# Kernel tuning notes

Hardware: AMD Instinct MI355X
Metric: run time of the kernel (lower is better)

Reference implementation:

```python
import jax, jax.numpy as jnp
import numpy as np

B, N, C = 4, 2048, 1024
H = 16
HD = C // H  # 64
THETA = 10000.0


def setup_inputs() -> dict:
    key = jax.random.key(0)
    k1, k2, k3, k4 = jax.random.split(key, 4)
    x = jax.random.normal(k1, (B, N, C), dtype=jnp.float32)
    # Linear-style init scaling to keep activations sane
    w_qkv = jax.random.normal(k2, (3 * C, C), dtype=jnp.float32) * (1.0 / np.sqrt(C))
    w_proj = jax.random.normal(k3, (C, C), dtype=jnp.float32) * (1.0 / np.sqrt(C))
    b_proj = jax.random.normal(k4, (C,), dtype=jnp.float32) * 0.01
    # RoPE frequencies: freqs_cis[n, j] = exp(i * n * theta^(-2j/hd))
    inv_freq = 1.0 / (THETA ** (jnp.arange(0, HD, 2, dtype=jnp.float32) / HD))  # (HD/2,)
    angles = jnp.arange(N, dtype=jnp.float32)[:, None] * inv_freq[None, :]  # (N, HD/2)
    freqs_cos = jnp.cos(angles)
    freqs_sin = jnp.sin(angles)
    return {"x": x, "w_qkv": w_qkv, "w_proj": w_proj, "b_proj": b_proj,
            "freqs_cos": freqs_cos, "freqs_sin": freqs_sin}


def _apply_rope(t, cos, sin):
    # t: (B, N, H, HD) -> complex pairs on last dim
    tr = t.reshape(t.shape[:-1] + (HD // 2, 2))
    a, b = tr[..., 0], tr[..., 1]
    c = cos[None, :, None, :]  # (1, N, 1, HD/2)
    s = sin[None, :, None, :]
    out = jnp.stack([a * c - b * s, a * s + b * c], axis=-1)
    return out.reshape(t.shape)


def reference(x, w_qkv, w_proj, b_proj, freqs_cos, freqs_sin):
    Bx, Nx, Cx = x.shape
    scale = HD ** -0.5
    qkv = jnp.einsum('bnc,dc->bnd', x, w_qkv)  # (B, N, 3C)
    qkv = qkv.reshape(Bx, Nx, 3, H, HD)
    q, k, v = qkv[:, :, 0], qkv[:, :, 1], qkv[:, :, 2]  # (B, N, H, HD)
    q = _apply_rope(q, freqs_cos, freqs_sin)
    k = _apply_rope(k, freqs_cos, freqs_sin)
    # (B, H, N, HD)
    q = q.transpose(0, 2, 1, 3)
    k = k.transpose(0, 2, 1, 3)
    v = v.transpose(0, 2, 1, 3)
    attn = jnp.einsum('bhnd,bhmd->bhnm', q, k) * scale
    attn = jax.nn.softmax(attn, axis=-1)
    out = jnp.einsum('bhnm,bhmd->bhnd', attn, v)  # (B, H, N, HD)
    out = out.transpose(0, 2, 1, 3).reshape(Bx, Nx, Cx)
    return jnp.einsum('bnc,dc->bnd', out, w_proj) + b_proj
```

## Files before the change

### kernel.cpp

```cpp
#include <hip/hip_runtime.h>
#include <hip/hip_bf16.h>
#include <stdint.h>

#define B_  4
#define N_  2048
#define C_  1024
#define H_  16
#define HD_ 64
#define M_  (B_*N_)
#define K3_ (3*C_)

typedef __bf16 bf16;
typedef __bf16 bf16x8 __attribute__((ext_vector_type(8)));
typedef __bf16 bf16x4 __attribute__((ext_vector_type(4)));
typedef float f32x4 __attribute__((ext_vector_type(4)));
typedef float f32x16 __attribute__((ext_vector_type(16)));

#if __has_builtin(__builtin_amdgcn_exp2f)
#define EXP2(x) __builtin_amdgcn_exp2f(x)
#else
#define EXP2(x) exp2f(x)
#endif

__global__ void castk3(const float* __restrict__ a, bf16* __restrict__ oa, int na4,
                       const float* __restrict__ b, bf16* __restrict__ ob, int nb4,
                       const float* __restrict__ c, bf16* __restrict__ oc, int nc4) {
    int total = na4 + nb4 + nc4;
    int stride = gridDim.x * blockDim.x;
    for (int i = blockIdx.x * blockDim.x + threadIdx.x; i < total; i += stride) {
        const float* src; bf16* dst; int j = i;
        if (j < na4)              { src = a; dst = oa; }
        else if ((j -= na4) < nb4){ src = b; dst = ob; }
        else                      { j -= nb4; src = c; dst = oc; }
        float4 v = reinterpret_cast<const float4*>(src)[j];
        bf16x4 o;
        o[0] = (bf16)v.x; o[1] = (bf16)v.y; o[2] = (bf16)v.z; o[3] = (bf16)v.w;
        *reinterpret_cast<bf16x4*>(dst + (size_t)j * 4) = o;
    }
}

__device__ __forceinline__ void gll16(const bf16* g, const bf16* l) {
    __builtin_amdgcn_global_load_lds(
        (const __attribute__((address_space(1))) void*)g,
        (__attribute__((address_space(3))) void*)l, 16, 0, 0);
}

__device__ __forceinline__ uint32_t pkbf(float a, float b) {
    union { bf16 h[2]; uint32_t u; } U;
    U.h[0] = (bf16)a; U.h[1] = (bf16)b;
    return U.u;
}

__device__ __forceinline__ uint32_t pkraw(bf16 a, bf16 b) {
    union { bf16 h[2]; uint32_t u; } U;
    U.h[0] = a; U.h[1] = b;
    return U.u;
}

template<int MODE>
__global__ __launch_bounds__(256, 4)
void gemm_bt(const bf16* __restrict__ A, const bf16* __restrict__ Bm,
             int Nn, int Kk,
             bf16* __restrict__ qout, bf16* __restrict__ kout, bf16* __restrict__ vout,
             const float* __restrict__ fcos, const float* __restrict__ fsin,
             const float* __restrict__ bias, float* __restrict__ Cout)
{
    __shared__ bf16 a_lds[2][128 * 32];
    __shared__ bf16 b_lds[2][128 * 32];
    const int tid  = threadIdx.x;
    const int lane = tid & 63;
    const int w    = tid >> 6;
    const int wr   = w >> 1, wc = w & 1;
    const int ntile = Nn >> 7;
    const int nwg = gridDim.x, cpx = nwg >> 3;
    const int swz = (blockIdx.x & 7) * cpx + (blockIdx.x >> 3);
    const int bx = swz % ntile, by = swz / ntile;
    const int m0 = by * 128, n0 = bx * 128;

    f32x4 acc[4][4] = {};

    const int c0 = tid, c1 = tid + 256;
    const bf16* ga0 = A  + (size_t)(m0 + (c0 >> 2)) * Kk + (c0 & 3) * 8;
    const bf16* ga1 = A  + (size_t)(m0 + (c1 >> 2)) * Kk + (c1 & 3) * 8;
    const bf16* gb0 = Bm + (size_t)(n0 + (c0 >> 2)) * Kk + (c0 & 3) * 8;
    const bf16* gb1 = Bm + (size_t)(n0 + (c1 >> 2)) * Kk + (c1 & 3) * 8;

    const int rA = lane & 15;
    const int kk = (lane >> 4) * 8;

    gll16(ga0, &a_lds[0][w * 512]);
    gll16(ga1, &a_lds[0][w * 512 + 2048]);
    gll16(gb0, &b_lds[0][w * 512]);
    gll16(gb1, &b_lds[0][w * 512 + 2048]);
    __syncthreads();

    for (int k0 = 0; k0 < Kk; k0 += 32) {
        const int cur = (k0 >> 5) & 1, nxt = cur ^ 1;
        if (k0 + 32 < Kk) {
            gll16(ga0 + k0 + 32, &a_lds[nxt][w * 512]);
            gll16(ga1 + k0 + 32, &a_lds[nxt][w * 512 + 2048]);
            gll16(gb0 + k0 + 32, &b_lds[nxt][w * 512]);
            gll16(gb1 + k0 + 32, &b_lds[nxt][w * 512 + 2048]);
        }

        bf16x8 af[4], bfr[4];
#pragma unroll
        for (int m = 0; m < 4; ++m)
            af[m] = *reinterpret_cast<const bf16x8*>(&a_lds[cur][(wr * 64 + m * 16 + rA) * 32 + kk]);
#pragma unroll
        for (int n = 0; n < 4; ++n)
            bfr[n] = *reinterpret_cast<const bf16x8*>(&b_lds[cur][(wc * 64 + n * 16 + rA) * 32 + kk]);
#pragma unroll
        for (int m = 0; m < 4; ++m)
#pragma unroll
            for (int n = 0; n < 4; ++n)
                acc[m][n] = __builtin_amdgcn_mfma_f32_16x16x32_bf16(af[m], bfr[n], acc[m][n], 0, 0, 0);
        __syncthreads();
    }

    if (MODE == 1) {
#pragma unroll
        for (int n = 0; n < 4; ++n) {
            int cg = n0 + wc * 64 + n * 16 + (lane & 15);
            float bv = bias[cg];
#pragma unroll
            for (int m = 0; m < 4; ++m) {
                int rg = m0 + wr * 64 + m * 16 + (lane >> 4) * 4;
#pragma unroll
                for (int r = 0; r < 4; ++r)
                    Cout[(size_t)(rg + r) * Nn + cg] = acc[m][n][r] + bv;
            }
        }
    } else {
        const int part = n0 >> 10;
#pragma unroll
        for (int n = 0; n < 4; ++n) {
            int cg  = n0 + wc * 64 + n * 16 + (lane & 15);
            int rem = cg & 1023;
            int h   = rem >> 6, hd = rem & 63;
#pragma unroll
            for (int m = 0; m < 4; ++m) {
#pragma unroll
                for (int r = 0; r < 4; ++r) {
                    int rg   = m0 + wr * 64 + m * 16 + (lane >> 4) * 4 + r;
                    int b    = rg >> 11, nrow = rg & 2047;
                    float val = acc[m][n][r];
                    size_t oi = ((size_t)(b * 16 + h) * N_ + nrow) * HD_ + hd;
                    if (part == 2) {
                        vout[oi] = (bf16)val;
                    } else {
                        float p   = __shfl_xor(val, 1);
                        float cth = fcos[nrow * 32 + (hd >> 1)];
                        float sth = fsin[nrow * 32 + (hd >> 1)];
                        float o   = (lane & 1) ? (val * cth + p * sth) : (val * cth - p * sth);
                        if (part == 0) { o *= 0.18033688011112042f; qout[oi] = (bf16)o; }
                        else           { kout[oi] = (bf16)o; }
                    }
                }
            }
        }
    }
}

#define NT_ (N_ / 64)
__global__ __launch_bounds__(256, 2)
void attn_kernel(const bf16* __restrict__ Q, const bf16* __restrict__ Kb,
                 const bf16* __restrict__ Vb, bf16* __restrict__ Ob)
{
    __shared__ bf16 k_lds[2][64 * 64];
    __shared__ bf16 vt_lds[2][64 * 64];
    const int tid = threadIdx.x, lane = tid & 63, w = tid >> 6;
    const int h5  = lane >> 5;
    const int l31 = lane & 31;
    const int nqt = N_ / 128;
    const int cpx = gridDim.x >> 3;
    const int swzb = (blockIdx.x & 7) * cpx + (blockIdx.x >> 3);
    const int bh = swzb / nqt, qt = swzb % nqt;
    const size_t base = (size_t)bh * N_ * HD_;
    const int q0 = qt * 128 + w * 32;

    bf16x8 qf[4];
    {
        const bf16* qp = Q + base + (size_t)(q0 + l31) * HD_ + h5 * 8;
#pragma unroll
        for (int t = 0; t < 4; ++t)
            qf[t] = *reinterpret_cast<const bf16x8*>(qp + t * 16);
    }

    f32x16 oT[2] = {};
    float l_run = 0.f;

    const int kRowA = tid >> 3;
    const int kColA = ((tid & 7) ^ (kRowA & 7)) * 8;
    const int kRowB = kRowA + 32;
    const int kColB = ((tid & 7) ^ (kRowB & 7)) * 8;
    const bf16* kSrcA = Kb + base + (size_t)kRowA * HD_ + kColA;
    const bf16* kSrcB = Kb + base + (size_t)kRowB * HD_ + kColB;

    const int kp = tid & 31, dc = tid >> 5;
    const bf16* vSrc0 = Vb + base + (size_t)(2 * kp) * HD_ + dc * 8;
    const bf16* vSrc1 = vSrc0 + HD_;

#define STORE_VT(bufidx, va, vb) do {                                              \
        char* vtb = reinterpret_cast<char*>(&vt_lds[0][0]) + (bufidx) * 8192;      \
        _Pragma("unroll")                                                          \
        for (int j = 0; j < 8; ++j) {                                              \
            int byteoff = (dc * 8 + j) * 128 + ((4 * kp) ^ (j << 4));              \
            *reinterpret_cast<uint32_t*>(vtb + byteoff) = pkraw((va)[j], (vb)[j]); \
        }                                                                          \
    } while (0)

    bf16x8 v0 = *reinterpret_cast<const bf16x8*>(vSrc0);
    bf16x8 v1 = *reinterpret_cast<const bf16x8*>(vSrc1);
    gll16(kSrcA, &k_lds[0][w * 512]);
    gll16(kSrcB, &k_lds[0][2048 + w * 512]);
    STORE_VT(0, v0, v1);
    __syncthreads();

    for (int it = 0; it < NT_; ++it) {
        const int cur = it & 1, nxt = cur ^ 1;
        const bool more = (it + 1 < NT_);

        if (more) {
            size_t adv = (size_t)(it + 1) * 64 * HD_;
            v0 = *reinterpret_cast<const bf16x8*>(vSrc0 + adv);
            v1 = *reinterpret_cast<const bf16x8*>(vSrc1 + adv);
            gll16(kSrcA + adv, &k_lds[nxt][w * 512]);
            gll16(kSrcB + adv, &k_lds[nxt][2048 + w * 512]);
        }

        const char* kbase  = reinterpret_cast<const char*>(&k_lds[0][0]) + cur * 8192;
        const char* vtbase = reinterpret_cast<const char*>(&vt_lds[0][0]) + cur * 8192;
        float psum = 0.f;

#pragma unroll
        for (int s = 0; s < 2; ++s) {
            f32x16 st = {};
            const int row = s * 32 + l31;
#pragma unroll
            for (int t = 0; t < 4; ++t) {
                int cc = (2 * t + h5) ^ (row & 7);
                bf16x8 kf = *reinterpret_cast<const bf16x8*>(kbase + row * 128 + cc * 16);
                st = __builtin_amdgcn_mfma_f32_32x32x16_bf16(kf, qf[t], st, 0, 0, 0);
            }

#pragma unroll
            for (int i = 0; i < 16; ++i)
                st[i] = EXP2(st[i]);

            float t8[8];
#pragma unroll
            for (int i = 0; i < 8; ++i) t8[i] = st[i] + st[i + 8];
#pragma unroll
            for (int i = 0; i < 4; ++i) t8[i] = t8[i] + t8[i + 4];
            psum += (t8[0] + t8[1]) + (t8[2] + t8[3]);

            uint32_t pk2[4][2];
#pragma unroll
            for (int g = 0; g < 4; ++g) {
                pk2[g][0] = pkbf(st[4 * g + 0], st[4 * g + 1]);
                pk2[g][1] = pkbf(st[4 * g + 2], st[4 * g + 3]);
            }
#pragma unroll
            for (int tt = 0; tt < 2; ++tt) {
                const int t = 2 * s + tt;
                uint32_t a0 = pk2[2 * tt][0], b0 = pk2[2 * tt + 1][0];
                uint32_t a1 = pk2[2 * tt][1], b1 = pk2[2 * tt + 1][1];
                asm volatile("v_permlane32_swap_b32 %0, %1" : "+v"(a0), "+v"(b0));
                asm volatile("v_permlane32_swap_b32 %0, %1" : "+v"(a1), "+v"(b1));
                union { uint32_t u[4]; bf16x8 v; } U;
                U.u[0] = a0; U.u[1] = a1; U.u[2] = b0; U.u[3] = b1;
#pragma unroll
                for (int n = 0; n < 2; ++n) {
                    int vrow = n * 32 + l31;
                    int cc   = (2 * t + h5) ^ (vrow & 7);
                    bf16x8 vf = *reinterpret_cast<const bf16x8*>(vtbase + vrow * 128 + cc * 16);
                    oT[n] = __builtin_amdgcn_mfma_f32_32x32x16_bf16(vf, U.v, oT[n], 0, 0, 0);
                }
            }

            if (s == 0 && more) STORE_VT(nxt, v0, v1);
        }

        psum += __shfl_xor(psum, 32);
        l_run += psum;

        __syncthreads();
    }

    const int b = bh >> 4, hh = bh & 15;
    float inv = 1.0f / l_run;
    int q = q0 + l31;
#pragma unroll
    for (int n = 0; n < 2; ++n)
#pragma unroll
        for (int g = 0; g < 4; ++g) {
            int d = n * 32 + 8 * g + 4 * h5;
            bf16x4 o4;
#pragma unroll
            for (int r = 0; r < 4; ++r) o4[r] = (bf16)(oT[n][4 * g + r] * inv);
            *reinterpret_cast<bf16x4*>(Ob + ((size_t)(b * N_ + q)) * C_ + hh * 64 + d) = o4;
        }
#undef STORE_VT
}

extern "C" void kernel_launch(void* const* d_in, const int* in_sizes, int n_in,
                              void* d_out, int out_size, void* d_ws, size_t ws_size,
                              hipStream_t stream) {
    const float* x     = (const float*)d_in[0];
    const float* wqkv  = (const float*)d_in[1];
    const float* wproj = (const float*)d_in[2];
    const float* bproj = (const float*)d_in[3];
    const float* fcos  = (const float*)d_in[4];
    const float* fsin  = (const float*)d_in[5];
    float* out = (float*)d_out;

    bf16* x_bf     = (bf16*)d_ws;
    bf16* wqkv_bf  = x_bf    + (size_t)M_ * C_;
    bf16* wproj_bf = wqkv_bf + (size_t)K3_ * C_;
    bf16* qbuf     = wproj_bf + (size_t)C_ * C_;
    bf16* kbuf     = qbuf  + (size_t)M_ * C_;
    bf16* vbuf     = kbuf  + (size_t)M_ * C_;
    bf16* abuf     = vbuf  + (size_t)M_ * C_;

    castk3<<<2048, 256, 0, stream>>>(x,     x_bf,     M_ * C_ / 4,
                                     wqkv,  wqkv_bf,  K3_ * C_ / 4,
                                     wproj, wproj_bf, C_ * C_ / 4);

    gemm_bt<0><<<64 * 24, 256, 0, stream>>>(x_bf, wqkv_bf, K3_, C_,
                                            qbuf, kbuf, vbuf, fcos, fsin, nullptr, nullptr);
    attn_kernel<<<64 * 16, 256, 0, stream>>>(qbuf, kbuf, vbuf, abuf);
    gemm_bt<1><<<64 * 8, 256, 0, stream>>>(abuf, wproj_bf, C_, C_,
                                           nullptr, nullptr, nullptr, nullptr, nullptr, bproj, out);
}
```

Measured before the change: 241.1 us.

## Process two 32-row query tiles per wave in attention to reuse K/V fragments

```diff
diff --git a/kernel.cpp b/kernel.cpp
--- a/kernel.cpp
+++ b/kernel.cpp
@@ -172,23 +172,24 @@
     const int tid = threadIdx.x, lane = tid & 63, w = tid >> 6;
     const int h5  = lane >> 5;
     const int l31 = lane & 31;
-    const int nqt = N_ / 128;
+    const int nqt = N_ / 256;
     const int cpx = gridDim.x >> 3;
     const int swzb = (blockIdx.x & 7) * cpx + (blockIdx.x >> 3);
     const int bh = swzb / nqt, qt = swzb % nqt;
     const size_t base = (size_t)bh * N_ * HD_;
-    const int q0 = qt * 128 + w * 32;
-
-    bf16x8 qf[4];
-    {
-        const bf16* qp = Q + base + (size_t)(q0 + l31) * HD_ + h5 * 8;
+    const int q0 = qt * 256 + w * 64;
+
+    bf16x8 qf[2][4];
+#pragma unroll
+    for (int h = 0; h < 2; ++h) {
+        const bf16* qp = Q + base + (size_t)(q0 + h * 32 + l31) * HD_ + h5 * 8;
 #pragma unroll
         for (int t = 0; t < 4; ++t)
-            qf[t] = *reinterpret_cast<const bf16x8*>(qp + t * 16);
-    }
-
-    f32x16 oT[2] = {};
-    float l_run = 0.f;
+            qf[h][t] = *reinterpret_cast<const bf16x8*>(qp + t * 16);
+    }
+
+    f32x16 oT[2][2] = {};
+    float l0 = 0.f, l1 = 0.f;
 
     const int kRowA = tid >> 3;
     const int kColA = ((tid & 7) ^ (kRowA & 7)) * 8;
@@ -231,76 +232,92 @@
 
         const char* kbase  = reinterpret_cast<const char*>(&k_lds[0][0]) + cur * 8192;
         const char* vtbase = reinterpret_cast<const char*>(&vt_lds[0][0]) + cur * 8192;
-        float psum = 0.f;
+        float psum0 = 0.f, psum1 = 0.f;
 
 #pragma unroll
         for (int s = 0; s < 2; ++s) {
-            f32x16 st = {};
+            f32x16 st0 = {}, st1 = {};
             const int row = s * 32 + l31;
 #pragma unroll
             for (int t = 0; t < 4; ++t) {
                 int cc = (2 * t + h5) ^ (row & 7);
                 bf16x8 kf = *reinterpret_cast<const bf16x8*>(kbase + row * 128 + cc * 16);
-                st = __builtin_amdgcn_mfma_f32_32x32x16_bf16(kf, qf[t], st, 0, 0, 0);
-            }
-
-#pragma unroll
-            for (int i = 0; i < 16; ++i)
-                st[i] = EXP2(st[i]);
-
-            float t8[8];
-#pragma unroll
-            for (int i = 0; i < 8; ++i) t8[i] = st[i] + st[i + 8];
-#pragma unroll
-            for (int i = 0; i < 4; ++i) t8[i] = t8[i] + t8[i + 4];
-            psum += (t8[0] + t8[1]) + (t8[2] + t8[3]);
-
-            uint32_t pk2[4][2];
+                st0 = __builtin_amdgcn_mfma_f32_32x32x16_bf16(kf, qf[0][t], st0, 0, 0, 0);
+                st1 = __builtin_amdgcn_mfma_f32_32x32x16_bf16(kf, qf[1][t], st1, 0, 0, 0);
+            }
+
+#pragma unroll
+            for (int i = 0; i < 16; ++i) st0[i] = EXP2(st0[i]);
+#pragma unroll
+            for (int i = 0; i < 16; ++i) st1[i] = EXP2(st1[i]);
+
+            float t8[8], u8[8];
+#pragma unroll
+            for (int i = 0; i < 8; ++i) { t8[i] = st0[i] + st0[i + 8]; u8[i] = st1[i] + st1[i + 8]; }
+#pragma unroll
+            for (int i = 0; i < 4; ++i) { t8[i] = t8[i] + t8[i + 4];   u8[i] = u8[i] + u8[i + 4]; }
+            psum0 += (t8[0] + t8[1]) + (t8[2] + t8[3]);
+            psum1 += (u8[0] + u8[1]) + (u8[2] + u8[3]);
+
+            uint32_t pk0[4][2], pk1[4][2];
 #pragma unroll
             for (int g = 0; g < 4; ++g) {
-                pk2[g][0] = pkbf(st[4 * g + 0], st[4 * g + 1]);
-                pk2[g][1] = pkbf(st[4 * g + 2], st[4 * g + 3]);
+                pk0[g][0] = pkbf(st0[4 * g + 0], st0[4 * g + 1]);
+                pk0[g][1] = pkbf(st0[4 * g + 2], st0[4 * g + 3]);
+                pk1[g][0] = pkbf(st1[4 * g + 0], st1[4 * g + 1]);
+                pk1[g][1] = pkbf(st1[4 * g + 2], st1[4 * g + 3]);
             }
 #pragma unroll
             for (int tt = 0; tt < 2; ++tt) {
                 const int t = 2 * s + tt;
-                uint32_t a0 = pk2[2 * tt][0], b0 = pk2[2 * tt + 1][0];
-                uint32_t a1 = pk2[2 * tt][1], b1 = pk2[2 * tt + 1][1];
+                uint32_t a0 = pk0[2 * tt][0], b0 = pk0[2 * tt + 1][0];
+                uint32_t a1 = pk0[2 * tt][1], b1 = pk0[2 * tt + 1][1];
+                uint32_t c0 = pk1[2 * tt][0], d0 = pk1[2 * tt + 1][0];
+                uint32_t c1 = pk1[2 * tt][1], d1 = pk1[2 * tt + 1][1];
                 asm volatile("v_permlane32_swap_b32 %0, %1" : "+v"(a0), "+v"(b0));
                 asm volatile("v_permlane32_swap_b32 %0, %1" : "+v"(a1), "+v"(b1));
-                union { uint32_t u[4]; bf16x8 v; } U;
-                U.u[0] = a0; U.u[1] = a1; U.u[2] = b0; U.u[3] = b1;
+                asm volatile("v_permlane32_swap_b32 %0, %1" : "+v"(c0), "+v"(d0));
+                asm volatile("v_permlane32_swap_b32 %0, %1" : "+v"(c1), "+v"(d1));
+                union { uint32_t u[4]; bf16x8 v; } U0, U1;
+                U0.u[0] = a0; U0.u[1] = a1; U0.u[2] = b0; U0.u[3] = b1;
+                U1.u[0] = c0; U1.u[1] = c1; U1.u[2] = d0; U1.u[3] = d1;
 #pragma unroll
                 for (int n = 0; n < 2; ++n) {
                     int vrow = n * 32 + l31;
                     int cc   = (2 * t + h5) ^ (vrow & 7);
                     bf16x8 vf = *reinterpret_cast<const bf16x8*>(vtbase + vrow * 128 + cc * 16);
-                    oT[n] = __builtin_amdgcn_mfma_f32_32x32x16_bf16(vf, U.v, oT[n], 0, 0, 0);
+                    oT[0][n] = __builtin_amdgcn_mfma_f32_32x32x16_bf16(vf, U0.v, oT[0][n], 0, 0, 0);
+                    oT[1][n] = __builtin_amdgcn_mfma_f32_32x32x16_bf16(vf, U1.v, oT[1][n], 0, 0, 0);
                 }
             }
 
             if (s == 0 && more) STORE_VT(nxt, v0, v1);
         }
 
-        psum += __shfl_xor(psum, 32);
-        l_run += psum;
+        psum0 += __shfl_xor(psum0, 32);
+        psum1 += __shfl_xor(psum1, 32);
+        l0 += psum0;
+        l1 += psum1;
 
         __syncthreads();
     }
 
     const int b = bh >> 4, hh = bh & 15;
-    float inv = 1.0f / l_run;
-    int q = q0 + l31;
-#pragma unroll
-    for (int n = 0; n < 2; ++n)
-#pragma unroll
-        for (int g = 0; g < 4; ++g) {
-            int d = n * 32 + 8 * g + 4 * h5;
-            bf16x4 o4;
-#pragma unroll
-            for (int r = 0; r < 4; ++r) o4[r] = (bf16)(oT[n][4 * g + r] * inv);
-            *reinterpret_cast<bf16x4*>(Ob + ((size_t)(b * N_ + q)) * C_ + hh * 64 + d) = o4;
-        }
+#pragma unroll
+    for (int h = 0; h < 2; ++h) {
+        float inv = 1.0f / (h ? l1 : l0);
+        int q = q0 + h * 32 + l31;
+#pragma unroll
+        for (int n = 0; n < 2; ++n)
+#pragma unroll
+            for (int g = 0; g < 4; ++g) {
+                int d = n * 32 + 8 * g + 4 * h5;
+                bf16x4 o4;
+#pragma unroll
+                for (int r = 0; r < 4; ++r) o4[r] = (bf16)(oT[h][n][4 * g + r] * inv);
+                *reinterpret_cast<bf16x4*>(Ob + ((size_t)(b * N_ + q)) * C_ + hh * 64 + d) = o4;
+            }
+    }
 #undef STORE_VT
 }
 
@@ -329,7 +346,7 @@
 
     gemm_bt<0><<<64 * 24, 256, 0, stream>>>(x_bf, wqkv_bf, K3_, C_,
                                             qbuf, kbuf, vbuf, fcos, fsin, nullptr, nullptr);
-    attn_kernel<<<64 * 16, 256, 0, stream>>>(qbuf, kbuf, vbuf, abuf);
+    attn_kernel<<<64 * 8, 256, 0, stream>>>(qbuf, kbuf, vbuf, abuf);
     gemm_bt<1><<<64 * 8, 256, 0, stream>>>(abuf, wproj_bf, C_, C_,
                                            nullptr, nullptr, nullptr, nullptr, nullptr, bproj, out);
 }
```

Result: faster. 218.9 us (-9.2%).
